# Kernel optimization log

Measured on AMD Instinct MI355X. Metric: run time of the kernel, lower is better.

Reference implementation:

```python
import jax, jax.numpy as jnp
import numpy as np

N_NODES = 50000   # n_all_entities
N_EDGES = 800000  # nnz of sparse A_in (avg degree 16)
D = 96            # in_dim == out_dim
NEG_SLOPE = 0.01  # nn.LeakyReLU default


def setup_inputs() -> dict:
    key = jax.random.key(0)
    ks = jax.random.split(key, 8)
    ego = jax.random.normal(ks[0], (N_NODES, D), dtype=jnp.float32)
    a_rows = jax.random.randint(ks[1], (N_EDGES,), 0, N_NODES)
    a_cols = jax.random.randint(ks[2], (N_EDGES,), 0, N_NODES)
    a_vals = jax.random.uniform(ks[3], (N_EDGES,), dtype=jnp.float32)
    # torch Linear weights: shape (out_dim, in_dim), xavier-like scale
    scale = np.sqrt(2.0 / (D + D)).astype(np.float32)
    W1 = jax.random.normal(ks[4], (D, D), dtype=jnp.float32) * scale
    b1 = jnp.zeros((D,), dtype=jnp.float32)
    W2 = jax.random.normal(ks[5], (D, D), dtype=jnp.float32) * scale
    b2 = jnp.zeros((D,), dtype=jnp.float32)
    return {"ego": ego, "a_vals": a_vals, "W1": W1, "b1": b1,
            "W2": W2, "b2": b2, "a_rows": a_rows, "a_cols": a_cols}


def _leaky_relu(x):
    return jnp.where(x >= 0, x, NEG_SLOPE * x)


def reference(ego, a_vals, W1, b1, W2, b2, a_rows, a_cols):
    # side = A_in @ ego  (sparse COO matmul via gather + segment_sum)
    msgs = a_vals[:, None] * ego[a_cols]                      # [E, D]
    side = jax.ops.segment_sum(msgs, a_rows, num_segments=N_NODES)  # [N, D]
    # bi-interaction aggregator (dropout is identity in eval mode)
    sum_emb = _leaky_relu((ego + side) @ W1.T + b1)           # [N, D]
    bi_emb = _leaky_relu((ego * side) @ W2.T + b2)            # [N, D]
    return sum_emb + bi_emb
```

## Files before the change

### kernel.cpp

```cpp
#include <hip/hip_runtime.h>

#define NN 50000
#define NE 800000
#define DD 96
#define NEG 0.01f
#define FN 64
#define XST 104
#define NBK 196
#define BCAP 4600
#define EPA 4096
#define NBA 196
#define OVCAP 65536
#define QROW 128

typedef __attribute__((ext_vector_type(8))) short short8v;
typedef __attribute__((ext_vector_type(4))) float f32x4;

static __device__ __forceinline__ float lrelu(float x) {
  return (x >= 0.f) ? x : NEG * x;
}
static __device__ __forceinline__ unsigned short f2bf(float x) {
  unsigned u = __float_as_uint(x);
  u += 0x7fffu + ((u >> 16) & 1u);
  return (unsigned short)(u >> 16);
}
static __device__ __forceinline__ float bf2f(unsigned short h) {
  return __uint_as_float(((unsigned)h) << 16);
}
static __device__ __forceinline__ float bflo(unsigned u) {
  return __uint_as_float(u << 16);
}
static __device__ __forceinline__ float bfhi(unsigned u) {
  return __uint_as_float(u & 0xFFFF0000u);
}
static __device__ __forceinline__ float sb(unsigned u, int k) {
  return (float)((int)(signed char)((u >> (8 * k)) & 0xFF));
}

__global__ __launch_bounds__(256) void scatter_kernel(
    const float* __restrict__ ego, const float* __restrict__ avals,
    const int* __restrict__ arows, const int* __restrict__ acols,
    float* __restrict__ side)
{
  int t = blockIdx.x * 256 + threadIdx.x;
  int e = t >> 5;
  int lane = t & 31;
  if (e >= NE) return;
  int row = arows[e];
  int col = acols[e];
  float v = avals[e];
  if (lane < 24) {
    const float4* src = (const float4*)(ego + (size_t)col * DD);
    float4 x = src[lane];
    float* dst = side + (size_t)row * DD + lane * 4;
    unsafeAtomicAdd(dst + 0, v * x.x);
    unsafeAtomicAdd(dst + 1, v * x.y);
    unsafeAtomicAdd(dst + 2, v * x.z);
    unsafeAtomicAdd(dst + 3, v * x.w);
  }
}

__global__ __launch_bounds__(192) void fuse_fb_kernel(
    const float* __restrict__ ego, const float* __restrict__ side,
    const float* __restrict__ W1, const float* __restrict__ b1,
    const float* __restrict__ W2, const float* __restrict__ b2,
    float* __restrict__ out)
{
  __shared__ float W1t[DD * DD];
  __shared__ float W2t[DD * DD];
  __shared__ float b1s[DD], b2s[DD];
  __shared__ float xs[192], ys[192];
  int tid = threadIdx.x;
  for (int i = tid; i < DD * DD; i += 192) {
    int j = i / DD, k = i - j * DD;
    W1t[k * DD + j] = W1[i];
    W2t[k * DD + j] = W2[i];
  }
  if (tid < DD) { b1s[tid] = b1[tid]; b2s[tid] = b2[tid]; }
  __syncthreads();
  int nl = tid / DD, j = tid - nl * DD;
  for (int p = blockIdx.x; p < NN / 2; p += gridDim.x) {
    int base = p * 192;
    float e = ego[base + tid], s = side[base + tid];
    xs[tid] = e + s; ys[tid] = e * s;
    __syncthreads();
    float a1 = b1s[j], a2 = b2s[j];
    const float* xr = xs + nl * DD;
    const float* yr = ys + nl * DD;
#pragma unroll 16
    for (int k = 0; k < DD; ++k) {
      a1 += xr[k] * W1t[k * DD + j];
      a2 += yr[k] * W2t[k * DD + j];
    }
    float r = lrelu(a1) + lrelu(a2);
    __syncthreads();
    out[base + tid] = r;
  }
}

#define NB_W   ((DD * DD) / 256)
#define NB_Q   ((NN + 63) / 64)
__global__ __launch_bounds__(256) void build_kernel(
    const int* __restrict__ rows, const int* __restrict__ cols,
    const float* __restrict__ vals,
    int* __restrict__ bptr, int* __restrict__ ovcur,
    int2* __restrict__ ovbuf, int2* __restrict__ buckets,
    const float* __restrict__ W1, const float* __restrict__ W2,
    unsigned short* __restrict__ Wb1, unsigned short* __restrict__ Wb2,
    const float* __restrict__ ego, unsigned char* __restrict__ egoq)
{
  __shared__ unsigned sw0[EPA];
  __shared__ unsigned sw1[EPA];
  __shared__ unsigned char sbid[EPA];
  __shared__ int bcnt[256], bofs[256], gbase[256], stmp[256];

  int blk = blockIdx.x;
  int tid = threadIdx.x;

  if (blk >= NBA) {
    int b = blk - NBA;
    if (b < NB_W) {
      int i = b * 256 + tid;
      Wb1[i] = f2bf(W1[i]);
      Wb2[i] = f2bf(W2[i]);
    } else {
      int r_loc = tid >> 2, q = tid & 3;
      int row = (b - NB_W) * 64 + r_loc;
      if (row < NN) {
        float4 f[6];
        const float4* src = (const float4*)(ego + (size_t)row * DD + q * 24);
#pragma unroll
        for (int t = 0; t < 6; ++t) f[t] = src[t];
        float m = 0.f;
#pragma unroll
        for (int t = 0; t < 6; ++t) {
          m = fmaxf(m, fmaxf(fmaxf(fabsf(f[t].x), fabsf(f[t].y)),
                             fmaxf(fabsf(f[t].z), fabsf(f[t].w))));
        }
        m = fmaxf(m, __shfl_xor(m, 1, 64));
        m = fmaxf(m, __shfl_xor(m, 2, 64));
        m = fmaxf(m, 1e-20f);
        float inv = 127.0f / m;
        unsigned* dst = (unsigned*)(egoq + (size_t)row * QROW) + q * 6;
#pragma unroll
        for (int t = 0; t < 6; ++t) {
          int q0 = __float2int_rn(f[t].x * inv);
          int q1 = __float2int_rn(f[t].y * inv);
          int q2 = __float2int_rn(f[t].z * inv);
          int q3 = __float2int_rn(f[t].w * inv);
          dst[t] = (unsigned)(q0 & 255) | ((unsigned)(q1 & 255) << 8) |
                   ((unsigned)(q2 & 255) << 16) | ((unsigned)(q3 & 255) << 24);
        }
        if (q == 0) *(float*)(egoq + (size_t)row * QROW + DD) = m * (1.0f / 127.0f);
      }
    }
    return;
  }

  int base = blk * EPA;
  int cnt_here = min(EPA, NE - base);

  bcnt[tid] = 0;
  __syncthreads();

  unsigned w0[16], w1[16];
  int bb[16], lp[16];
#pragma unroll
  for (int k = 0; k < 16; ++k) {
    int i = tid + k * 256;
    bb[k] = -1;
    if (i < cnt_here) {
      int e = base + i;
      int r = rows[e], c = cols[e];
      float v = vals[e];
      int b = r >> 8;
      bb[k] = b;
      w0[k] = (unsigned)c | ((unsigned)(r & 255) << 16) | ((unsigned)b << 24);
      w1[k] = (unsigned)f2bf(v);
      lp[k] = atomicAdd(&bcnt[b], 1);
    }
  }
  __syncthreads();

  int v = bcnt[tid];
  stmp[tid] = v;
  __syncthreads();
  for (int off = 1; off < 256; off <<= 1) {
    int add = (tid >= off) ? stmp[tid - off] : 0;
    __syncthreads();
    stmp[tid] += add;
    __syncthreads();
  }
  bofs[tid] = stmp[tid] - v;
  gbase[tid] = (tid < NBK && v > 0) ? atomicAdd(&bptr[tid], v) : 0;
  __syncthreads();

#pragma unroll
  for (int k = 0; k < 16; ++k) {
    if (bb[k] >= 0) {
      int s = bofs[bb[k]] + lp[k];
      sw0[s] = w0[k];
      sw1[s] = w1[k];
      sbid[s] = (unsigned char)bb[k];
    }
  }
  __syncthreads();

  for (int i = tid; i < cnt_here; i += 256) {
    int b = sbid[i];
    int off = i - bofs[b];
    int g = gbase[b] + off;
    int2 ent = make_int2((int)sw0[i], (int)sw1[i]);
    if (g < BCAP) {
      buckets[(size_t)b * BCAP + g] = ent;
    } else {
      int op = atomicAdd(ovcur, 1);
      if (op < OVCAP) ovbuf[op] = ent;
    }
  }
}

__global__ __launch_bounds__(256) void binB_kernel(
    const int2* __restrict__ buckets, const int* __restrict__ bptr,
    const int* __restrict__ ovcur, const int2* __restrict__ ovbuf,
    unsigned* __restrict__ cv, int* __restrict__ row_start)
{
  __shared__ int2 sent[BCAP];
  __shared__ int rcnt[256], rofs[256], rcur[256], stmp[256], sexc[256];
  int b = blockIdx.x, tid = threadIdx.x;

  int bv = (tid < NBK) ? bptr[tid] : 0;
  stmp[tid] = bv;
  __syncthreads();
  for (int off = 1; off < 256; off <<= 1) {
    int add = (tid >= off) ? stmp[tid - off] : 0;
    __syncthreads();
    stmp[tid] += add;
    __syncthreads();
  }
  sexc[tid] = stmp[tid] - bv;
  __syncthreads();
  int cvb = sexc[b];
  int total = bptr[b];
  int nreg = min(total, BCAP);
  int nov = min(*ovcur, OVCAP);
  const int2* reg = buckets + (size_t)b * BCAP;

  rcnt[tid] = 0;
  for (int i = tid; i < nreg; i += 256) sent[i] = reg[i];
  __syncthreads();

  for (int i = tid; i < nreg; i += 256) {
    unsigned w0 = (unsigned)sent[i].x;
    atomicAdd(&rcnt[(w0 >> 16) & 255], 1);
  }
  for (int i = tid; i < nov; i += 256) {
    unsigned w0 = (unsigned)ovbuf[i].x;
    if ((w0 >> 24) == (unsigned)b) atomicAdd(&rcnt[(w0 >> 16) & 255], 1);
  }
  __syncthreads();

  int v = rcnt[tid];
  stmp[tid] = v;
  __syncthreads();
  for (int off = 1; off < 256; off <<= 1) {
    int add = (tid >= off) ? stmp[tid - off] : 0;
    __syncthreads();
    stmp[tid] += add;
    __syncthreads();
  }
  rofs[tid] = stmp[tid] - v;
  rcur[tid] = rofs[tid];
  int grow = b * 256 + tid;
  if (grow <= NN) row_start[grow] = cvb + rofs[tid];
  __syncthreads();

  for (int i = tid; i < nreg; i += 256) {
    unsigned w0 = (unsigned)sent[i].x;
    unsigned w1 = (unsigned)sent[i].y;
    int rl = (w0 >> 16) & 255;
    int p = atomicAdd(&rcur[rl], 1);
    cv[cvb + p] = (w0 & 0xFFFFu) | (w1 << 16);
  }
  for (int i = tid; i < nov; i += 256) {
    unsigned w0 = (unsigned)ovbuf[i].x;
    unsigned w1 = (unsigned)ovbuf[i].y;
    if ((w0 >> 24) == (unsigned)b) {
      int rl = (w0 >> 16) & 255;
      int p = atomicAdd(&rcur[rl], 1);
      cv[cvb + p] = (w0 & 0xFFFFu) | (w1 << 16);
    }
  }
}

__global__ __launch_bounds__(256) void agg_kernel(
    const unsigned char* __restrict__ egoq, const int* __restrict__ row_start,
    const unsigned* __restrict__ cv, unsigned* __restrict__ sideb) {
  int wid = threadIdx.x >> 6, lane = threadIdx.x & 63;
  int row = blockIdx.x * 4 + wid;
  if (row >= NN) return;
  int s = row_start[row], e = row_start[row + 1];
  int q = lane >> 4, ql = lane & 15;
  bool act = ql < 12;
  int ql8 = ql * 8;

  float a[4][8];
#pragma unroll
  for (int d = 0; d < 4; ++d)
#pragma unroll
    for (int j = 0; j < 8; ++j) a[d][j] = 0.f;

  for (int base = s; base < e; base += 64) {
    int idx = base + lane;
    unsigned pk = 0;
    if (idx < e) pk = cv[idx];
    int n = min(64, e - base);
    for (int i = 0; i < n; i += 16) {
      unsigned p[4];
#pragma unroll
      for (int d = 0; d < 4; ++d) p[d] = __shfl(pk, i + 4 * d + q, 64);
      uint2 u[4];
      float sc[4];
#pragma unroll
      for (int d = 0; d < 4; ++d) {
        const char* rowp = (const char*)egoq + ((size_t)(p[d] & 0xFFFFu) << 7);
        if (act) {
          u[d] = *(const uint2*)(rowp + ql8);
          sc[d] = *(const float*)(rowp + DD);
        } else {
          u[d] = make_uint2(0u, 0u);
          sc[d] = 0.f;
        }
      }
#pragma unroll
      for (int d = 0; d < 4; ++d) {
        float vs = bfhi(p[d]) * sc[d];
        a[d][0] += vs * sb(u[d].x, 0);
        a[d][1] += vs * sb(u[d].x, 1);
        a[d][2] += vs * sb(u[d].x, 2);
        a[d][3] += vs * sb(u[d].x, 3);
        a[d][4] += vs * sb(u[d].y, 0);
        a[d][5] += vs * sb(u[d].y, 1);
        a[d][6] += vs * sb(u[d].y, 2);
        a[d][7] += vs * sb(u[d].y, 3);
      }
    }
  }

  float r[8];
#pragma unroll
  for (int j = 0; j < 8; ++j) {
    r[j] = (a[0][j] + a[1][j]) + (a[2][j] + a[3][j]);
    r[j] += __shfl_xor(r[j], 16, 64);
    r[j] += __shfl_xor(r[j], 32, 64);
  }
  if (q == 0 && act) {
    uint4 o;
    o.x = (unsigned)f2bf(r[0]) | ((unsigned)f2bf(r[1]) << 16);
    o.y = (unsigned)f2bf(r[2]) | ((unsigned)f2bf(r[3]) << 16);
    o.z = (unsigned)f2bf(r[4]) | ((unsigned)f2bf(r[5]) << 16);
    o.w = (unsigned)f2bf(r[6]) | ((unsigned)f2bf(r[7]) << 16);
    *(uint4*)(sideb + (size_t)row * 48 + ql * 4) = o;
  }
}

__global__ __launch_bounds__(256) void fuse4_kernel(
    const unsigned char* __restrict__ egoq, const unsigned* __restrict__ sideb,
    const unsigned short* __restrict__ Wb1, const unsigned short* __restrict__ Wb2,
    const float* __restrict__ b1, const float* __restrict__ b2,
    float* __restrict__ out)
{
  __shared__ unsigned short xs[FN * XST];
  __shared__ unsigned short ys[FN * XST];
  int tid = threadIdx.x;
  int nbase = blockIdx.x * FN;

  for (int i = tid; i < FN * 24; i += 256) {
    int r = i / 24, u = i - r * 24;
    float e0 = 0.f, e1 = 0.f, e2 = 0.f, e3 = 0.f;
    float s0 = 0.f, s1 = 0.f, s2 = 0.f, s3 = 0.f;
    if (nbase + r < NN) {
      const char* rowp = (const char*)egoq + ((size_t)(nbase + r) << 7);
      float sc = *(const float*)(rowp + DD);
      unsigned uq = *(const unsigned*)(rowp + u * 4);
      e0 = sc * sb(uq, 0);
      e1 = sc * sb(uq, 1);
      e2 = sc * sb(uq, 2);
      e3 = sc * sb(uq, 3);
      uint2 sv = *(const uint2*)(sideb + (size_t)(nbase + r) * 48 + u * 2);
      s0 = bflo(sv.x); s1 = bfhi(sv.x);
      s2 = bflo(sv.y); s3 = bfhi(sv.y);
    }
    unsigned xlo = (unsigned)f2bf(e0 + s0) | ((unsigned)f2bf(e1 + s1) << 16);
    unsigned xhi = (unsigned)f2bf(e2 + s2) | ((unsigned)f2bf(e3 + s3) << 16);
    unsigned ylo = (unsigned)f2bf(e0 * s0) | ((unsigned)f2bf(e1 * s1) << 16);
    unsigned yhi = (unsigned)f2bf(e2 * s2) | ((unsigned)f2bf(e3 * s3) << 16);
    *(uint2*)(xs + r * XST + u * 4) = make_uint2(xlo, xhi);
    *(uint2*)(ys + r * XST + u * 4) = make_uint2(ylo, yhi);
  }
  __syncthreads();

  int w = tid >> 6, l = tid & 63;
  int lrow = l & 15, lk = l >> 4;

  f32x4 acc1[6], acc2[6];
#pragma unroll
  for (int t = 0; t < 6; ++t) {
    acc1[t] = (f32x4){0.f, 0.f, 0.f, 0.f};
    acc2[t] = (f32x4){0.f, 0.f, 0.f, 0.f};
  }

  const unsigned short* xrow = xs + (w * 16 + lrow) * XST + lk * 8;
  const unsigned short* yrow = ys + (w * 16 + lrow) * XST + lk * 8;

#pragma unroll
  for (int kk = 0; kk < 3; ++kk) {
    short8v ax = *(const short8v*)(xrow + kk * 32);
    short8v ay = *(const short8v*)(yrow + kk * 32);
    int kb = kk * 32 + lk * 8;
#pragma unroll
    for (int t = 0; t < 6; ++t) {
      int j = t * 16 + lrow;
      short8v bw1 = *(const short8v*)(Wb1 + j * DD + kb);
      short8v bw2 = *(const short8v*)(Wb2 + j * DD + kb);
      acc1[t] = __builtin_amdgcn_mfma_f32_16x16x32_bf16(ax, bw1, acc1[t], 0, 0, 0);
      acc2[t] = __builtin_amdgcn_mfma_f32_16x16x32_bf16(ay, bw2, acc2[t], 0, 0, 0);
    }
  }

  int node0 = nbase + w * 16 + lk * 4;
#pragma unroll
  for (int t = 0; t < 6; ++t) {
    int j = t * 16 + lrow;
    float bb1 = b1[j], bb2 = b2[j];
#pragma unroll
    for (int i = 0; i < 4; ++i) {
      int node = node0 + i;
      if (node < NN)
        out[(size_t)node * DD + j] = lrelu(acc1[t][i] + bb1) + lrelu(acc2[t][i] + bb2);
    }
  }
}

extern "C" void kernel_launch(void* const* d_in, const int* in_sizes, int n_in,
                              void* d_out, int out_size, void* d_ws, size_t ws_size,
                              hipStream_t stream) {
  const float* ego   = (const float*)d_in[0];
  const float* avals = (const float*)d_in[1];
  const float* W1    = (const float*)d_in[2];
  const float* b1    = (const float*)d_in[3];
  const float* W2    = (const float*)d_in[4];
  const float* b2    = (const float*)d_in[5];
  const int* arows   = (const int*)d_in[6];
  const int* acols   = (const int*)d_in[7];
  float* out = (float*)d_out;

  size_t off = 0;
  auto bump = [&](size_t bytes) {
    size_t o = off;
    off += (bytes + 1023) & ~(size_t)1023;
    return o;
  };
  char* ws = (char*)d_ws;
  size_t o_rs    = bump((size_t)(NN + 1) * 4);
  size_t o_cv    = bump((size_t)NE * 4);
  size_t o_wb1   = bump((size_t)DD * DD * 2);
  size_t o_wb2   = bump((size_t)DD * DD * 2);
  size_t o_egoq  = bump((size_t)NN * QROW);
  size_t o_bptr  = bump((size_t)(NBK + 1) * 4);
  size_t o_ovbuf = bump((size_t)OVCAP * 8);
  size_t o_sideb = bump((size_t)NN * DD * 2);
  size_t need = off;
  static_assert((size_t)NBK * BCAP * 8 <= (size_t)NN * DD * 2, "buckets fit in sideb");

  if (ws_size >= need) {
    int*  rs    = (int*)(ws + o_rs);
    unsigned* cv = (unsigned*)(ws + o_cv);
    unsigned short* Wb1  = (unsigned short*)(ws + o_wb1);
    unsigned short* Wb2  = (unsigned short*)(ws + o_wb2);
    unsigned char* egoq  = (unsigned char*)(ws + o_egoq);
    int*  bptr  = (int*)(ws + o_bptr);
    int*  ovcur = bptr + NBK;
    int2* ovbuf = (int2*)(ws + o_ovbuf);
    unsigned* sideb = (unsigned*)(ws + o_sideb);
    int2* buckets = (int2*)(ws + o_sideb);

    hipMemsetAsync(bptr, 0, (size_t)(NBK + 1) * 4, stream);
    build_kernel<<<NBA + NB_W + NB_Q, 256, 0, stream>>>(
        arows, acols, avals, bptr, ovcur, ovbuf, buckets,
        W1, W2, Wb1, Wb2, ego, egoq);
    binB_kernel<<<NBK, 256, 0, stream>>>(buckets, bptr, ovcur, ovbuf, cv, rs);
    agg_kernel<<<(NN + 3) / 4, 256, 0, stream>>>(egoq, rs, cv, sideb);
    fuse4_kernel<<<(NN + FN - 1) / FN, 256, 0, stream>>>(
        egoq, sideb, Wb1, Wb2, b1, b2, out);
  } else {
    size_t side_bytes = (size_t)NN * DD * sizeof(float);
    float* side = (ws_size >= side_bytes) ? (float*)d_ws : out;
    hipMemsetAsync(side, 0, side_bytes, stream);
    long long nthreads = (long long)NE * 32;
    int blocks = (int)((nthreads + 255) / 256);
    scatter_kernel<<<blocks, 256, 0, stream>>>(ego, avals, arows, acols, side);
    fuse_fb_kernel<<<1024, 192, 0, stream>>>(ego, side, W1, b1, W2, b2, out);
  }
}
```

Before: 83.91 us.

## Split int8 row scales into separate array and load MFMA operands directly from global

Quantized ego rows shrink from a 128-byte stride with an inline scale to a packed 96-byte stride, and the per-row scales move into a separate float array. The aggregation gather now reads the scale from that array rather than from the row tail. The fused GEMM kernel drops its LDS staging of x/y tiles and builds each lane's bf16 MFMA operands in registers straight from global egoq and side. The smaller layout cuts gather footprint, at the price of an extra scalar load per neighbor and rows that no longer align to 128 bytes.

```diff
diff --git a/kernel.cpp b/kernel.cpp
--- a/kernel.cpp
+++ b/kernel.cpp
@@ -5,13 +5,12 @@
 #define DD 96
 #define NEG 0.01f
 #define FN 64
-#define XST 104
 #define NBK 196
 #define BCAP 4600
 #define EPA 4096
 #define NBA 196
 #define OVCAP 65536
-#define QROW 128
+#define QROW 96
 
 typedef __attribute__((ext_vector_type(8))) short short8v;
 typedef __attribute__((ext_vector_type(4))) float f32x4;
@@ -23,9 +22,6 @@
   unsigned u = __float_as_uint(x);
   u += 0x7fffu + ((u >> 16) & 1u);
   return (unsigned short)(u >> 16);
-}
-static __device__ __forceinline__ float bf2f(unsigned short h) {
-  return __uint_as_float(((unsigned)h) << 16);
 }
 static __device__ __forceinline__ float bflo(unsigned u) {
   return __uint_as_float(u << 16);
@@ -107,7 +103,8 @@
     int2* __restrict__ ovbuf, int2* __restrict__ buckets,
     const float* __restrict__ W1, const float* __restrict__ W2,
     unsigned short* __restrict__ Wb1, unsigned short* __restrict__ Wb2,
-    const float* __restrict__ ego, unsigned char* __restrict__ egoq)
+    const float* __restrict__ ego, unsigned char* __restrict__ egoq,
+    float* __restrict__ scl)
 {
   __shared__ unsigned sw0[EPA];
   __shared__ unsigned sw1[EPA];
@@ -151,7 +148,7 @@
           dst[t] = (unsigned)(q0 & 255) | ((unsigned)(q1 & 255) << 8) |
                    ((unsigned)(q2 & 255) << 16) | ((unsigned)(q3 & 255) << 24);
         }
-        if (q == 0) *(float*)(egoq + (size_t)row * QROW + DD) = m * (1.0f / 127.0f);
+        if (q == 0) scl[row] = m * (1.0f / 127.0f);
       }
     }
     return;
@@ -294,8 +291,9 @@
 }
 
 __global__ __launch_bounds__(256) void agg_kernel(
-    const unsigned char* __restrict__ egoq, const int* __restrict__ row_start,
-    const unsigned* __restrict__ cv, unsigned* __restrict__ sideb) {
+    const unsigned char* __restrict__ egoq, const float* __restrict__ scl,
+    const int* __restrict__ row_start, const unsigned* __restrict__ cv,
+    unsigned* __restrict__ sideb) {
   int wid = threadIdx.x >> 6, lane = threadIdx.x & 63;
   int row = blockIdx.x * 4 + wid;
   if (row >= NN) return;
@@ -323,10 +321,11 @@
       float sc[4];
 #pragma unroll
       for (int d = 0; d < 4; ++d) {
-        const char* rowp = (const char*)egoq + ((size_t)(p[d] & 0xFFFFu) << 7);
+        int c = (int)(p[d] & 0xFFFFu);
+        const char* rowp = (const char*)egoq + (size_t)c * QROW;
         if (act) {
           u[d] = *(const uint2*)(rowp + ql8);
-          sc[d] = *(const float*)(rowp + DD);
+          sc[d] = scl[c];
         } else {
           u[d] = make_uint2(0u, 0u);
           sc[d] = 0.f;
@@ -365,43 +364,44 @@
 }
 
 __global__ __launch_bounds__(256) void fuse4_kernel(
-    const unsigned char* __restrict__ egoq, const unsigned* __restrict__ sideb,
+    const unsigned char* __restrict__ egoq, const float* __restrict__ scl,
+    const unsigned* __restrict__ sideb,
     const unsigned short* __restrict__ Wb1, const unsigned short* __restrict__ Wb2,
     const float* __restrict__ b1, const float* __restrict__ b2,
     float* __restrict__ out)
 {
-  __shared__ unsigned short xs[FN * XST];
-  __shared__ unsigned short ys[FN * XST];
   int tid = threadIdx.x;
-  int nbase = blockIdx.x * FN;
-
-  for (int i = tid; i < FN * 24; i += 256) {
-    int r = i / 24, u = i - r * 24;
-    float e0 = 0.f, e1 = 0.f, e2 = 0.f, e3 = 0.f;
-    float s0 = 0.f, s1 = 0.f, s2 = 0.f, s3 = 0.f;
-    if (nbase + r < NN) {
-      const char* rowp = (const char*)egoq + ((size_t)(nbase + r) << 7);
-      float sc = *(const float*)(rowp + DD);
-      unsigned uq = *(const unsigned*)(rowp + u * 4);
-      e0 = sc * sb(uq, 0);
-      e1 = sc * sb(uq, 1);
-      e2 = sc * sb(uq, 2);
-      e3 = sc * sb(uq, 3);
-      uint2 sv = *(const uint2*)(sideb + (size_t)(nbase + r) * 48 + u * 2);
-      s0 = bflo(sv.x); s1 = bfhi(sv.x);
-      s2 = bflo(sv.y); s3 = bfhi(sv.y);
-    }
-    unsigned xlo = (unsigned)f2bf(e0 + s0) | ((unsigned)f2bf(e1 + s1) << 16);
-    unsigned xhi = (unsigned)f2bf(e2 + s2) | ((unsigned)f2bf(e3 + s3) << 16);
-    unsigned ylo = (unsigned)f2bf(e0 * s0) | ((unsigned)f2bf(e1 * s1) << 16);
-    unsigned yhi = (unsigned)f2bf(e2 * s2) | ((unsigned)f2bf(e3 * s3) << 16);
-    *(uint2*)(xs + r * XST + u * 4) = make_uint2(xlo, xhi);
-    *(uint2*)(ys + r * XST + u * 4) = make_uint2(ylo, yhi);
-  }
-  __syncthreads();
-
   int w = tid >> 6, l = tid & 63;
   int lrow = l & 15, lk = l >> 4;
+  int nbase = blockIdx.x * FN;
+  int node = nbase + w * 16 + lrow;
+  bool valid = node < NN;
+  int nc = valid ? node : (NN - 1);
+
+  float sc = scl[nc];
+  short8v ax[3], ay[3];
+#pragma unroll
+  for (int kk = 0; kk < 3; ++kk) {
+    int kb = kk * 32 + lk * 8;
+    uint2 eu = *(const uint2*)(egoq + (size_t)nc * QROW + kb);
+    uint4 sv = *(const uint4*)(sideb + (size_t)nc * 48 + kb / 2);
+    float ev[8], svf[8];
+    ev[0] = sc * sb(eu.x, 0); ev[1] = sc * sb(eu.x, 1);
+    ev[2] = sc * sb(eu.x, 2); ev[3] = sc * sb(eu.x, 3);
+    ev[4] = sc * sb(eu.y, 0); ev[5] = sc * sb(eu.y, 1);
+    ev[6] = sc * sb(eu.y, 2); ev[7] = sc * sb(eu.y, 3);
+    svf[0] = bflo(sv.x); svf[1] = bfhi(sv.x);
+    svf[2] = bflo(sv.y); svf[3] = bfhi(sv.y);
+    svf[4] = bflo(sv.z); svf[5] = bfhi(sv.z);
+    svf[6] = bflo(sv.w); svf[7] = bfhi(sv.w);
+#pragma unroll
+    for (int i = 0; i < 8; ++i) {
+      float xv = valid ? (ev[i] + svf[i]) : 0.f;
+      float yv = valid ? (ev[i] * svf[i]) : 0.f;
+      ax[kk][i] = (short)f2bf(xv);
+      ay[kk][i] = (short)f2bf(yv);
+    }
+  }
 
   f32x4 acc1[6], acc2[6];
 #pragma unroll
@@ -410,21 +410,16 @@
     acc2[t] = (f32x4){0.f, 0.f, 0.f, 0.f};
   }
 
-  const unsigned short* xrow = xs + (w * 16 + lrow) * XST + lk * 8;
-  const unsigned short* yrow = ys + (w * 16 + lrow) * XST + lk * 8;
-
 #pragma unroll
   for (int kk = 0; kk < 3; ++kk) {
-    short8v ax = *(const short8v*)(xrow + kk * 32);
-    short8v ay = *(const short8v*)(yrow + kk * 32);
     int kb = kk * 32 + lk * 8;
 #pragma unroll
     for (int t = 0; t < 6; ++t) {
       int j = t * 16 + lrow;
       short8v bw1 = *(const short8v*)(Wb1 + j * DD + kb);
       short8v bw2 = *(const short8v*)(Wb2 + j * DD + kb);
-      acc1[t] = __builtin_amdgcn_mfma_f32_16x16x32_bf16(ax, bw1, acc1[t], 0, 0, 0);
-      acc2[t] = __builtin_amdgcn_mfma_f32_16x16x32_bf16(ay, bw2, acc2[t], 0, 0, 0);
+      acc1[t] = __builtin_amdgcn_mfma_f32_16x16x32_bf16(ax[kk], bw1, acc1[t], 0, 0, 0);
+      acc2[t] = __builtin_amdgcn_mfma_f32_16x16x32_bf16(ay[kk], bw2, acc2[t], 0, 0, 0);
     }
   }
 
@@ -435,9 +430,9 @@
     float bb1 = b1[j], bb2 = b2[j];
 #pragma unroll
     for (int i = 0; i < 4; ++i) {
-      int node = node0 + i;
-      if (node < NN)
-        out[(size_t)node * DD + j] = lrelu(acc1[t][i] + bb1) + lrelu(acc2[t][i] + bb2);
+      int n2 = node0 + i;
+      if (n2 < NN)
+        out[(size_t)n2 * DD + j] = lrelu(acc1[t][i] + bb1) + lrelu(acc2[t][i] + bb2);
     }
   }
 }
@@ -467,6 +462,7 @@
   size_t o_wb1   = bump((size_t)DD * DD * 2);
   size_t o_wb2   = bump((size_t)DD * DD * 2);
   size_t o_egoq  = bump((size_t)NN * QROW);
+  size_t o_scl   = bump((size_t)NN * 4);
   size_t o_bptr  = bump((size_t)(NBK + 1) * 4);
   size_t o_ovbuf = bump((size_t)OVCAP * 8);
   size_t o_sideb = bump((size_t)NN * DD * 2);
@@ -479,6 +475,7 @@
     unsigned short* Wb1  = (unsigned short*)(ws + o_wb1);
     unsigned short* Wb2  = (unsigned short*)(ws + o_wb2);
     unsigned char* egoq  = (unsigned char*)(ws + o_egoq);
+    float* scl  = (float*)(ws + o_scl);
     int*  bptr  = (int*)(ws + o_bptr);
     int*  ovcur = bptr + NBK;
     int2* ovbuf = (int2*)(ws + o_ovbuf);
@@ -488,11 +485,11 @@
     hipMemsetAsync(bptr, 0, (size_t)(NBK + 1) * 4, stream);
     build_kernel<<<NBA + NB_W + NB_Q, 256, 0, stream>>>(
         arows, acols, avals, bptr, ovcur, ovbuf, buckets,
-        W1, W2, Wb1, Wb2, ego, egoq);
+        W1, W2, Wb1, Wb2, ego, egoq, scl);
     binB_kernel<<<NBK, 256, 0, stream>>>(buckets, bptr, ovcur, ovbuf, cv, rs);
-    agg_kernel<<<(NN + 3) / 4, 256, 0, stream>>>(egoq, rs, cv, sideb);
+    agg_kernel<<<(NN + 3) / 4, 256, 0, stream>>>(egoq, scl, rs, cv, sideb);
     fuse4_kernel<<<(NN + FN - 1) / FN, 256, 0, stream>>>(
-        egoq, sideb, Wb1, Wb2, b1, b2, out);
+        egoq, scl, sideb, Wb1, Wb2, b1, b2, out);
   } else {
     size_t side_bytes = (size_t)NN * DD * sizeof(float);
     float* side = (ws_size >= side_bytes) ? (float*)d_ws : out;
```

New measurement: 85.99 us. +2.5%, slower.
